# Performance work log

Hardware: AMD Instinct MI355X
Metric: run time of the kernel (lower is better)

The kernel has to match this reference:

```python
import jax, jax.numpy as jnp
import numpy as np

OBS_RADIUS = 1.0
N = 8192      # num_agents
IN_DIM = 4    # state dim: [x, y, vx, vy]
HID = 64


def setup_inputs() -> dict:
    key = jax.random.key(0)
    ks = jax.random.split(key, 6)
    states = jax.random.normal(ks[0], (N, IN_DIM), dtype=jnp.float32)
    W1 = jax.random.normal(ks[1], (IN_DIM, HID), dtype=jnp.float32) / np.sqrt(IN_DIM).astype(np.float32)
    b1 = jnp.zeros((HID,), jnp.float32)
    W2 = jax.random.normal(ks[2], (HID, HID), dtype=jnp.float32) / np.sqrt(HID).astype(np.float32)
    b2 = jnp.zeros((HID,), jnp.float32)
    cw = jax.random.normal(ks[3], (HID,), dtype=jnp.float32) / np.sqrt(HID).astype(np.float32)  # Conv1d(64,1,1) weight
    cb = jnp.zeros((1,), jnp.float32)
    return {"states": states, "W1": W1, "b1": b1, "W2": W2, "b2": b2, "cw": cw, "cb": cb}


def _build_norm_adj(states):
    # radius graph on first two coords (positions); no self edges in the edge list,
    # GCNConv then adds self-loops and does symmetric D^-1/2 (A+I) D^-1/2 normalization.
    pos = states[:, :2]
    d2 = jnp.sum((pos[:, None, :] - pos[None, :, :]) ** 2, axis=-1)  # [N, N]
    mask = d2 <= jnp.asarray(OBS_RADIUS ** 2, states.dtype)          # [N, N] bool (incl. diagonal)
    eye = jnp.eye(N, dtype=bool)
    A_hat = jnp.where(mask & ~eye, jnp.asarray(1.0, states.dtype), 0.0) + jnp.eye(N, dtype=states.dtype)
    dinv = jax.lax.rsqrt(jnp.sum(A_hat, axis=1))                     # deg >= 1 (self loop)
    A_norm = dinv[:, None] * A_hat * dinv[None, :]
    return A_norm, mask


def reference(states, W1, b1, W2, b2, cw, cb):
    A_norm, mask = _build_norm_adj(states)
    # GCNConv 1: aggregate(normalized adj) of X W, plus bias, ReLU
    h = jax.nn.relu(A_norm @ (states @ W1) + b1)   # [N, 64]
    # GCNConv 2
    h = jax.nn.relu(A_norm @ (h @ W2) + b2)        # [N, 64]
    # Conv1d(64 -> 1, kernel=1): pointwise linear over channels
    out = h @ cw[:, None] + cb                     # [N, 1]
    return out, mask
```

## Files before the change

kernel.cpp:

```cpp
#include <hip/hip_runtime.h>
#include <hip/hip_bf16.h>
#include <stdint.h>

#define NPTS 8192

typedef float f32x4 __attribute__((ext_vector_type(4)));
typedef short s16x8 __attribute__((ext_vector_type(8)));

__device__ __forceinline__ unsigned short f2bf(float f) {
    unsigned int u = __builtin_bit_cast(unsigned int, f);
    u += 0x7FFFu + ((u >> 16) & 1u);
    return (unsigned short)(u >> 16);
}


__global__ __launch_bounds__(256) void k_mask(const float* __restrict__ states,
                                              const float* __restrict__ W1,
                                              float* __restrict__ mout,
                                              unsigned long long* __restrict__ maskb,
                                              float* __restrict__ dinv,
                                              uint4* __restrict__ y1) {
    __shared__ float xs[NPTS];
    __shared__ float ys[NPTS];
    __shared__ float dls[16];
    int tid = threadIdx.x;
    for (int r = tid; r < NPTS; r += 256) {
        float4 s = ((const float4*)states)[r];
        xs[r] = s.x; ys[r] = s.y;
    }
    __syncthreads();
    int wv = tid >> 6, L = tid & 63;
    int rowbase = blockIdx.x * 16 + wv * 4;
    float xi[4], yi[4];
    int deg[4] = {0, 0, 0, 0};
#pragma unroll
    for (int rr = 0; rr < 4; ++rr) { xi[rr] = xs[rowbase + rr]; yi[rr] = ys[rowbase + rr]; }
    for (int it = 0; it < 128; ++it) {
        int j = it * 64 + L;
        float xj = xs[j], yj = ys[j];
#pragma unroll
        for (int rr = 0; rr < 4; ++rr) {
            float dx = xi[rr] - xj;
            float dy = yi[rr] - yj;
            float d2 = __fadd_rn(__fmul_rn(dx, dx), __fmul_rn(dy, dy));
            bool pred = (d2 <= 1.0f);
            __builtin_nontemporal_store(pred ? 1.0f : 0.0f,
                                        &mout[(size_t)(rowbase + rr) * NPTS + j]);
            unsigned long long b = __ballot(pred);
            if (L == 0) maskb[(size_t)(rowbase + rr) * 128 + it] = b;
            deg[rr] += (int)__popcll(b);
        }
    }
    if (L == 0) {
#pragma unroll
        for (int rr = 0; rr < 4; ++rr) {
            float dv = rsqrtf((float)deg[rr]);
            dinv[rowbase + rr] = dv;
            dls[wv * 4 + rr] = dv;
        }
    }
    __syncthreads();
    if (tid < 128) {
        int ql = tid >> 6;
        int ct = (tid >> 4) & 3;
        int nn = tid & 15;
        int col = ct * 16 + nn;
        float w0 = W1[col], w1 = W1[64 + col], w2 = W1[128 + col], w3 = W1[192 + col];
        unsigned short frag[8];
#pragma unroll
        for (int t = 0; t < 8; ++t) {
            int rloc = ql * 8 + t;
            int k = blockIdx.x * 16 + rloc;
            float4 s = ((const float4*)states)[k];
            float acc = s.x * w0 + s.y * w1 + s.z * w2 + s.w * w3;
            frag[t] = f2bf(dls[rloc] * acc);
        }
        uint4 u;
        u.x = (unsigned)frag[0] | ((unsigned)frag[1] << 16);
        u.y = (unsigned)frag[2] | ((unsigned)frag[3] << 16);
        u.z = (unsigned)frag[4] | ((unsigned)frag[5] << 16);
        u.w = (unsigned)frag[6] | ((unsigned)frag[7] << 16);
        int kb = blockIdx.x >> 1;
        int quad = ql + 2 * (blockIdx.x & 1);
        y1[(kb * 4 + ct) * 64 + quad * 16 + nn] = u;
    }
}

__device__ __forceinline__ void agg_core(const uint4* __restrict__ y,
                                         const unsigned int* __restrict__ maskb,
                                         const float* __restrict__ dinv,
                                         const float* __restrict__ bias,
                                         float* __restrict__ redbuf,
                                         float* __restrict__ hbuf,
                                         int R0) {
    int tid = threadIdx.x;
    int w = tid >> 6, L = tid & 63;
    int n = L & 15, quad = L >> 4;
    const unsigned int* mrow0 = maskb + (size_t)(R0 + n) * 256 + w * 32;
    const unsigned int* mrow1 = mrow0 + 16 * 256;
    const uint4* yb = y + (size_t)w * 8192 + L;

    f32x4 acc[2][4] = {{{0,0,0,0},{0,0,0,0},{0,0,0,0},{0,0,0,0}},
                       {{0,0,0,0},{0,0,0,0},{0,0,0,0},{0,0,0,0}}};
    uint4 bcur[4];
    unsigned int mw0 = mrow0[0], mw1 = mrow1[0];
#pragma unroll
    for (int ct = 0; ct < 4; ++ct) bcur[ct] = yb[ct * 64];

    for (int kk = 0; kk < 32; ++kk) {
        uint4 bnext[4];
        unsigned int mwn0 = 0, mwn1 = 0;
        if (kk < 31) {
            const uint4* p = yb + (kk + 1) * 256;
#pragma unroll
            for (int ct = 0; ct < 4; ++ct) bnext[ct] = p[ct * 64];
            mwn0 = mrow0[kk + 1]; mwn1 = mrow1[kk + 1];
        }
        unsigned int by0 = (mw0 >> (quad * 8)) & 0xFFu;
        unsigned int by1 = (mw1 >> (quad * 8)) & 0xFFu;
        s16x8 a0, a1;
#pragma unroll
        for (int t = 0; t < 8; ++t) {
            a0[t] = (short)(((by0 >> t) & 1u) ? 0x3F80 : 0);
            a1[t] = (short)(((by1 >> t) & 1u) ? 0x3F80 : 0);
        }
#pragma unroll
        for (int ct = 0; ct < 4; ++ct) {
            s16x8 b = __builtin_bit_cast(s16x8, bcur[ct]);
            acc[0][ct] = __builtin_amdgcn_mfma_f32_16x16x32_bf16(a0, b, acc[0][ct], 0, 0, 0);
            acc[1][ct] = __builtin_amdgcn_mfma_f32_16x16x32_bf16(a1, b, acc[1][ct], 0, 0, 0);
        }
#pragma unroll
        for (int ct = 0; ct < 4; ++ct) bcur[ct] = bnext[ct];
        mw0 = mwn0; mw1 = mwn1;
    }
    float* rb = redbuf + w * 2048;
#pragma unroll
    for (int g = 0; g < 2; ++g)
#pragma unroll
        for (int ct = 0; ct < 4; ++ct)
#pragma unroll
            for (int r = 0; r < 4; ++r)
                rb[(g * 16 + quad * 4 + r) * 64 + ct * 16 + n] = acc[g][ct][r];
    __syncthreads();
    for (int e = tid; e < 2048; e += 512) {
        float z = 0.0f;
#pragma unroll
        for (int ww = 0; ww < 8; ++ww) z += redbuf[ww * 2048 + e];
        int row = e >> 6, col = e & 63;
        hbuf[row * 66 + col] = fmaxf(dinv[R0 + row] * z + bias[col], 0.0f);
    }
    __syncthreads();
}

__global__ __launch_bounds__(512) void k_layer1(const uint4* __restrict__ y1,
                                                const unsigned int* __restrict__ maskb,
                                                const float* __restrict__ dinv,
                                                const float* __restrict__ b1,
                                                const float* __restrict__ W2,
                                                uint4* __restrict__ y2) {
    __shared__ float redbuf[8 * 2048];
    __shared__ float hbuf[32 * 66];
    __shared__ float w2s[4096];
    int tid = threadIdx.x;
    for (int s = tid; s < 4096; s += 512) w2s[s] = W2[s];
    int R0 = blockIdx.x * 32;
    agg_core(y1, maskb, dinv, b1, redbuf, hbuf, R0);
    if (tid < 256) {
        int nn = tid & 15, q = (tid >> 4) & 3, ct = tid >> 6;
        int col = ct * 16 + nn;
        float dot[8] = {0, 0, 0, 0, 0, 0, 0, 0};
        for (int m = 0; m < 64; ++m) {
            float wv = w2s[m * 64 + col];
#pragma unroll
            for (int t = 0; t < 8; ++t)
                dot[t] = fmaf(hbuf[(q * 8 + t) * 66 + m], wv, dot[t]);
        }
        unsigned short v[8];
#pragma unroll
        for (int t = 0; t < 8; ++t) v[t] = f2bf(dinv[R0 + q * 8 + t] * dot[t]);
        uint4 u;
        u.x = (unsigned)v[0] | ((unsigned)v[1] << 16);
        u.y = (unsigned)v[2] | ((unsigned)v[3] << 16);
        u.z = (unsigned)v[4] | ((unsigned)v[5] << 16);
        u.w = (unsigned)v[6] | ((unsigned)v[7] << 16);
        y2[(blockIdx.x * 4 + ct) * 64 + q * 16 + nn] = u;
    }
}

__global__ __launch_bounds__(512) void k_layer2(const uint4* __restrict__ y2,
                                                const unsigned int* __restrict__ maskb,
                                                const float* __restrict__ dinv,
                                                const float* __restrict__ b2,
                                                const float* __restrict__ cw,
                                                const float* __restrict__ cb,
                                                float* __restrict__ out) {
    __shared__ float redbuf[8 * 2048];
    __shared__ float hbuf[32 * 66];
    __shared__ float cws[64];
    int tid = threadIdx.x;
    if (tid < 64) cws[tid] = cw[tid];
    int R0 = blockIdx.x * 32;
    agg_core(y2, maskb, dinv, b2, redbuf, hbuf, R0);
    int row = tid >> 4, cg = tid & 15;
    float v = 0.0f;
#pragma unroll
    for (int e = 0; e < 4; ++e) {
        int c = cg * 4 + e;
        v = fmaf(hbuf[row * 66 + c], cws[c], v);
    }
    v += __shfl_down(v, 8);
    v += __shfl_down(v, 4);
    v += __shfl_down(v, 2);
    v += __shfl_down(v, 1);
    if (cg == 0) out[R0 + row] = v + cb[0];
}

extern "C" void kernel_launch(void* const* d_in, const int* in_sizes, int n_in,
                              void* d_out, int out_size, void* d_ws, size_t ws_size,
                              hipStream_t stream) {
    const float* states = (const float*)d_in[0];
    const float* W1 = (const float*)d_in[1];
    const float* b1 = (const float*)d_in[2];
    const float* W2 = (const float*)d_in[3];
    const float* b2 = (const float*)d_in[4];
    const float* cw = (const float*)d_in[5];
    const float* cb = (const float*)d_in[6];
    float* out = (float*)d_out;
    float* mout = out + NPTS;

    char* ws = (char*)d_ws;
    float* dinv               = (float*)(ws);
    unsigned long long* maskb = (unsigned long long*)(ws + (1 << 16));
    uint4* y1                 = (uint4*)(ws + (1 << 16) + (8 << 20));
    uint4* y2                 = (uint4*)(ws + (1 << 16) + (9 << 20));

    hipLaunchKernelGGL(k_mask,   dim3(512), dim3(256), 0, stream,
                       states, W1, mout, maskb, dinv, y1);
    hipLaunchKernelGGL(k_layer1, dim3(256), dim3(512), 0, stream,
                       y1, (const unsigned int*)maskb, dinv, b1, W2, y2);
    hipLaunchKernelGGL(k_layer2, dim3(256), dim3(512), 0, stream,
                       y2, (const unsigned int*)maskb, dinv, b2, cw, cb, out);
}
```

Measured before the change: 350.0 us.

## Stage mask rows in LDS, double-buffer B loads, split W2 epilogue across all threads

The 32-row bitmask tile for each block is copied cooperatively into padded LDS, replacing per-lane strided global loads of mask words inside the MFMA loop. The K loop is unrolled by two with a two-deep register prefetch of the y fragments so global loads run further ahead of the MFMAs. The layer-1 h@W2 epilogue now uses all 512 threads, each doing half the rows and writing uint2 halves. The cost is about 33KB more LDS per block, which may lower occupancy, plus more registers for the extra prefetch buffers.

```diff
diff --git a/kernel.cpp b/kernel.cpp
--- a/kernel.cpp
+++ b/kernel.cpp
@@ -3,6 +3,7 @@
 #include <stdint.h>
 
 #define NPTS 8192
+#define MSTRIDE 260
 
 typedef float f32x4 __attribute__((ext_vector_type(4)));
 typedef short s16x8 __attribute__((ext_vector_type(8)));
@@ -91,48 +92,83 @@
                                          const float* __restrict__ dinv,
                                          const float* __restrict__ bias,
                                          float* __restrict__ redbuf,
+                                         unsigned int* __restrict__ mlds,
                                          float* __restrict__ hbuf,
                                          int R0) {
     int tid = threadIdx.x;
+    {
+        const uint4* src = (const uint4*)(maskb + (size_t)R0 * 256);
+        for (int e = tid; e < 2048; e += 512) {
+            uint4 v = src[e];
+            int r = e >> 6, c4 = e & 63;
+            *(uint4*)(mlds + r * MSTRIDE + c4 * 4) = v;
+        }
+    }
+    __syncthreads();
     int w = tid >> 6, L = tid & 63;
     int n = L & 15, quad = L >> 4;
-    const unsigned int* mrow0 = maskb + (size_t)(R0 + n) * 256 + w * 32;
-    const unsigned int* mrow1 = mrow0 + 16 * 256;
+    const unsigned int* mr0 = mlds + n * MSTRIDE + w * 32;
+    const unsigned int* mr1 = mr0 + 16 * MSTRIDE;
     const uint4* yb = y + (size_t)w * 8192 + L;
 
     f32x4 acc[2][4] = {{{0,0,0,0},{0,0,0,0},{0,0,0,0},{0,0,0,0}},
                        {{0,0,0,0},{0,0,0,0},{0,0,0,0},{0,0,0,0}}};
-    uint4 bcur[4];
-    unsigned int mw0 = mrow0[0], mw1 = mrow1[0];
-#pragma unroll
-    for (int ct = 0; ct < 4; ++ct) bcur[ct] = yb[ct * 64];
-
-    for (int kk = 0; kk < 32; ++kk) {
-        uint4 bnext[4];
-        unsigned int mwn0 = 0, mwn1 = 0;
-        if (kk < 31) {
-            const uint4* p = yb + (kk + 1) * 256;
-#pragma unroll
-            for (int ct = 0; ct < 4; ++ct) bnext[ct] = p[ct * 64];
-            mwn0 = mrow0[kk + 1]; mwn1 = mrow1[kk + 1];
-        }
-        unsigned int by0 = (mw0 >> (quad * 8)) & 0xFFu;
-        unsigned int by1 = (mw1 >> (quad * 8)) & 0xFFu;
-        s16x8 a0, a1;
-#pragma unroll
-        for (int t = 0; t < 8; ++t) {
-            a0[t] = (short)(((by0 >> t) & 1u) ? 0x3F80 : 0);
-            a1[t] = (short)(((by1 >> t) & 1u) ? 0x3F80 : 0);
-        }
-#pragma unroll
-        for (int ct = 0; ct < 4; ++ct) {
-            s16x8 b = __builtin_bit_cast(s16x8, bcur[ct]);
-            acc[0][ct] = __builtin_amdgcn_mfma_f32_16x16x32_bf16(a0, b, acc[0][ct], 0, 0, 0);
-            acc[1][ct] = __builtin_amdgcn_mfma_f32_16x16x32_bf16(a1, b, acc[1][ct], 0, 0, 0);
-        }
-#pragma unroll
-        for (int ct = 0; ct < 4; ++ct) bcur[ct] = bnext[ct];
-        mw0 = mwn0; mw1 = mwn1;
+    uint4 b0[4], b1[4];
+#pragma unroll
+    for (int ct = 0; ct < 4; ++ct) b0[ct] = yb[ct * 64];
+#pragma unroll
+    for (int ct = 0; ct < 4; ++ct) b1[ct] = yb[256 + ct * 64];
+
+    for (int kk = 0; kk < 32; kk += 2) {
+        uint4 bn[4];
+        if (kk + 2 < 32) {
+            const uint4* p = yb + (kk + 2) * 256;
+#pragma unroll
+            for (int ct = 0; ct < 4; ++ct) bn[ct] = p[ct * 64];
+        }
+        {
+            unsigned int mw0 = mr0[kk], mw1 = mr1[kk];
+            unsigned int by0 = (mw0 >> (quad * 8)) & 0xFFu;
+            unsigned int by1 = (mw1 >> (quad * 8)) & 0xFFu;
+            s16x8 a0, a1;
+#pragma unroll
+            for (int t = 0; t < 8; ++t) {
+                a0[t] = (short)(((by0 >> t) & 1u) ? 0x3F80 : 0);
+                a1[t] = (short)(((by1 >> t) & 1u) ? 0x3F80 : 0);
+            }
+#pragma unroll
+            for (int ct = 0; ct < 4; ++ct) {
+                s16x8 b = __builtin_bit_cast(s16x8, b0[ct]);
+                acc[0][ct] = __builtin_amdgcn_mfma_f32_16x16x32_bf16(a0, b, acc[0][ct], 0, 0, 0);
+                acc[1][ct] = __builtin_amdgcn_mfma_f32_16x16x32_bf16(a1, b, acc[1][ct], 0, 0, 0);
+            }
+        }
+#pragma unroll
+        for (int ct = 0; ct < 4; ++ct) b0[ct] = bn[ct];
+        if (kk + 3 < 32) {
+            const uint4* p = yb + (kk + 3) * 256;
+#pragma unroll
+            for (int ct = 0; ct < 4; ++ct) bn[ct] = p[ct * 64];
+        }
+        {
+            unsigned int mw0 = mr0[kk + 1], mw1 = mr1[kk + 1];
+            unsigned int by0 = (mw0 >> (quad * 8)) & 0xFFu;
+            unsigned int by1 = (mw1 >> (quad * 8)) & 0xFFu;
+            s16x8 a0, a1;
+#pragma unroll
+            for (int t = 0; t < 8; ++t) {
+                a0[t] = (short)(((by0 >> t) & 1u) ? 0x3F80 : 0);
+                a1[t] = (short)(((by1 >> t) & 1u) ? 0x3F80 : 0);
+            }
+#pragma unroll
+            for (int ct = 0; ct < 4; ++ct) {
+                s16x8 b = __builtin_bit_cast(s16x8, b1[ct]);
+                acc[0][ct] = __builtin_amdgcn_mfma_f32_16x16x32_bf16(a0, b, acc[0][ct], 0, 0, 0);
+                acc[1][ct] = __builtin_amdgcn_mfma_f32_16x16x32_bf16(a1, b, acc[1][ct], 0, 0, 0);
+            }
+        }
+#pragma unroll
+        for (int ct = 0; ct < 4; ++ct) b1[ct] = bn[ct];
     }
     float* rb = redbuf + w * 2048;
 #pragma unroll
@@ -160,31 +196,31 @@
                                                 const float* __restrict__ W2,
                                                 uint4* __restrict__ y2) {
     __shared__ float redbuf[8 * 2048];
+    __shared__ unsigned int mlds[32 * MSTRIDE];
     __shared__ float hbuf[32 * 66];
     __shared__ float w2s[4096];
     int tid = threadIdx.x;
     for (int s = tid; s < 4096; s += 512) w2s[s] = W2[s];
     int R0 = blockIdx.x * 32;
-    agg_core(y1, maskb, dinv, b1, redbuf, hbuf, R0);
-    if (tid < 256) {
-        int nn = tid & 15, q = (tid >> 4) & 3, ct = tid >> 6;
+    agg_core(y1, maskb, dinv, b1, redbuf, mlds, hbuf, R0);
+    {
+        int nn = tid & 15, q = (tid >> 4) & 3, ct = (tid >> 6) & 3, half = tid >> 8;
         int col = ct * 16 + nn;
-        float dot[8] = {0, 0, 0, 0, 0, 0, 0, 0};
+        float dot[4] = {0, 0, 0, 0};
         for (int m = 0; m < 64; ++m) {
             float wv = w2s[m * 64 + col];
 #pragma unroll
-            for (int t = 0; t < 8; ++t)
-                dot[t] = fmaf(hbuf[(q * 8 + t) * 66 + m], wv, dot[t]);
-        }
-        unsigned short v[8];
-#pragma unroll
-        for (int t = 0; t < 8; ++t) v[t] = f2bf(dinv[R0 + q * 8 + t] * dot[t]);
-        uint4 u;
+            for (int t = 0; t < 4; ++t)
+                dot[t] = fmaf(hbuf[(q * 8 + half * 4 + t) * 66 + m], wv, dot[t]);
+        }
+        unsigned short v[4];
+#pragma unroll
+        for (int t = 0; t < 4; ++t) v[t] = f2bf(dinv[R0 + q * 8 + half * 4 + t] * dot[t]);
+        uint2 u;
         u.x = (unsigned)v[0] | ((unsigned)v[1] << 16);
         u.y = (unsigned)v[2] | ((unsigned)v[3] << 16);
-        u.z = (unsigned)v[4] | ((unsigned)v[5] << 16);
-        u.w = (unsigned)v[6] | ((unsigned)v[7] << 16);
-        y2[(blockIdx.x * 4 + ct) * 64 + q * 16 + nn] = u;
+        int fragidx = (blockIdx.x * 4 + ct) * 64 + q * 16 + nn;
+        ((uint2*)y2)[fragidx * 2 + half] = u;
     }
 }
 
@@ -196,12 +232,13 @@
                                                 const float* __restrict__ cb,
                                                 float* __restrict__ out) {
     __shared__ float redbuf[8 * 2048];
+    __shared__ unsigned int mlds[32 * MSTRIDE];
     __shared__ float hbuf[32 * 66];
     __shared__ float cws[64];
     int tid = threadIdx.x;
     if (tid < 64) cws[tid] = cw[tid];
     int R0 = blockIdx.x * 32;
-    agg_core(y2, maskb, dinv, b2, redbuf, hbuf, R0);
+    agg_core(y2, maskb, dinv, b2, redbuf, mlds, hbuf, R0);
     int row = tid >> 4, cg = tid & 15;
     float v = 0.0f;
 #pragma unroll
```

Result: faster. 334.7 us (median of 2 runs) (-4.4%).
